# Performance work log

Hardware: AMD Instinct MI355X
Metric: run time of the kernel (lower is better)

Reference implementation:

```python
import jax, jax.numpy as jnp
import numpy as np

N = 50000
H = 8          # heads
C = 10         # out channels per head
F_IN = 128
NEG_SLOPE = 0.2


def _glorot(key, shape, fan_in):
    return jax.random.normal(key, shape, dtype=jnp.float32) / np.sqrt(fan_in)


def setup_inputs() -> dict:
    key = jax.random.key(0)
    ks = jax.random.split(key, 16)
    x = jax.random.normal(ks[0], (N, F_IN), dtype=jnp.float32)
    edge_index = jax.random.randint(ks[1], (2, 1600000), 0, N, dtype=jnp.int64)
    inp = {"x": x, "edge_index": edge_index}
    dims = [F_IN, H * C, H * C]  # input dim of each of the 3 layers
    k = 2
    for i, din in enumerate(dims):
        inp[f"Wl{i}"] = _glorot(ks[k + 0], (din, H * C), din)
        inp[f"Wr{i}"] = _glorot(ks[k + 1], (din, H * C), din)
        inp[f"att{i}"] = _glorot(ks[k + 2], (H, C), C)
        inp[f"b{i}"] = jnp.zeros((H * C,), dtype=jnp.float32)
        k += 3
    return inp


def gatv2_layer(x, Wl, Wr, att, b, src, dst):
    # GATv2Conv (PyG defaults): separate lin_l/lin_r, e = att . leaky_relu(xl_j + xr_i),
    # segment softmax over incoming edges, scatter-add of alpha * xl_j, concat heads + bias.
    n = x.shape[0]
    xl = (x @ Wl).reshape(n, H, C)
    xr = (x @ Wr).reshape(n, H, C)
    e = jax.nn.leaky_relu(xl[src] + xr[dst], NEG_SLOPE)      # [E, H, C]
    score = jnp.einsum('ehc,hc->eh', e, att)                 # [E, H]
    smax = jax.ops.segment_max(score, dst, num_segments=n)   # [N, H]
    ex = jnp.exp(score - smax[dst])
    denom = jax.ops.segment_sum(ex, dst, num_segments=n)
    alpha = ex / (denom[dst] + 1e-16)                        # [E, H]
    out = jax.ops.segment_sum(alpha[:, :, None] * xl[src], dst, num_segments=n)
    return out.reshape(n, H * C) + b


def reference(x, edge_index, Wl0, Wr0, att0, b0, Wl1, Wr1, att1, b1, Wl2, Wr2, att2, b2):
    n = x.shape[0]
    # add_self_loops=True (PyG default)
    loop = jnp.arange(n, dtype=edge_index.dtype)
    src = jnp.concatenate([edge_index[0], loop])
    dst = jnp.concatenate([edge_index[1], loop])
    params = [(Wl0, Wr0, att0, b0), (Wl1, Wr1, att1, b1), (Wl2, Wr2, att2, b2)]
    for Wl, Wr, att, b in params:
        x = jax.nn.elu(gatv2_layer(x, Wl, Wr, att, b, src, dst))
    return x
```

## Files before the change

kernel.cpp:

```cpp
#include <hip/hip_runtime.h>
#include <hip/hip_bf16.h>
#include <hip/hip_fp16.h>

#define N_NODES 50000
#define HEADS 8
#define CHANS 10
#define HC 80
#define PADH 12
#define PHL 96
#define F_IN 128
#define E_EDGES 1600000
#define E_TOT (E_EDGES + N_NODES)
#define NEG_SLOPE 0.2f
#define NBUCK 3125
#define NCHUNK 128
#define CHUNK ((E_TOT + NCHUNK - 1) / NCHUNK)
#define XS_STRIDE 40
#define WS_STRIDE 40

typedef _Float16 f16x8 __attribute__((ext_vector_type(8)));
typedef float f32x4 __attribute__((ext_vector_type(4)));

#if __has_builtin(__builtin_amdgcn_fdot2) && __has_builtin(__builtin_elementwise_max)
#define USE_PK 1
typedef _Float16 h2 __attribute__((ext_vector_type(2)));
#else
#define USE_PK 0
#endif

__device__ inline void load_edge(const void* ei, int is64, int e, int& src, int& dst) {
    if (e < E_EDGES) {
        if (is64) {
            src = ((const int*)ei)[2 * e];
            dst = ((const int*)ei)[2 * (E_EDGES + e)];
        } else {
            src = ((const int*)ei)[e];
            dst = ((const int*)ei)[E_EDGES + e];
        }
    } else {
        src = dst = e - E_EDGES;
    }
}

__device__ inline int load_dst(const void* ei, int is64, int e) {
    if (e < E_EDGES) {
        if (is64) return ((const int*)ei)[2 * (E_EDGES + e)];
        return ((const int*)ei)[E_EDGES + e];
    }
    return e - E_EDGES;
}

__device__ inline int detect_is64(const void* ei, int tid, int* s_flag) {
    if (tid < 64) {
        const int* p = (const int*)ei;
        bool ok = (p[2 * tid + 1] == 0) && (p[2 * (tid + 64) + 1] == 0);
        unsigned long long m = __ballot(ok);
        if (tid == 0) *s_flag = (m == ~0ull) ? 1 : 0;
    }
    return 0;
}

__global__ __launch_bounds__(256) void hist_wconv_kernel(
        const void* ei, int* __restrict__ hist, int* __restrict__ bcount,
        const float* __restrict__ Wl0, const float* __restrict__ Wr0,
        const float* __restrict__ Wl1, const float* __restrict__ Wr1,
        const float* __restrict__ Wl2, const float* __restrict__ Wr2,
        __half* __restrict__ wt) {
    int blk = blockIdx.x;
    int tid = threadIdx.x;
    if (blk >= NCHUNK) {
        if (tid < 128) {
            int g = blk - NCHUNK;
            int layer = g / 160, c = g - layer * 160;
            int kp = tid;
            const float* Wl = (layer == 0) ? Wl0 : (layer == 1) ? Wl1 : Wl2;
            const float* Wr = (layer == 0) ? Wr0 : (layer == 1) ? Wr1 : Wr2;
            const float* W = (c < 80) ? Wl : Wr;
            int cc = (c < 80) ? c : c - 80;
            float v = 0.f;
            if (layer == 0) {
                if (kp < F_IN) v = W[kp * 80 + cc];
            } else {
                int hh = kp / PADH, c2 = kp - hh * PADH;
                if (kp < PHL && c2 < CHANS)
                    v = W[(hh * CHANS + c2) * 80 + cc];
            }
            wt[(size_t)g * 128 + kp] = __float2half_rn(v);
        }
        return;
    }
    __shared__ int h[NBUCK];
    __shared__ int s_is64;
    for (int i = tid; i < NBUCK; i += 256) h[i] = 0;
    detect_is64(ei, tid, &s_is64);
    __syncthreads();
    int is64 = s_is64;
    int e0 = blk * CHUNK, e1 = min(e0 + CHUNK, E_TOT);
    for (int e = e0 + tid; e < e1; e += 4 * 256) {
        int d[4]; int cnt = 0;
        #pragma unroll
        for (int u = 0; u < 4; u++) {
            int ee = e + u * 256;
            if (ee < e1) { d[u] = load_dst(ei, is64, ee); cnt = u + 1; }
        }
        #pragma unroll
        for (int u = 0; u < 4; u++)
            if (u < cnt) atomicAdd(&h[d[u] >> 4], 1);
    }
    __syncthreads();
    for (int i = tid; i < NBUCK; i += 256) {
        int v = h[i];
        int old = v ? atomicAdd(&bcount[i], v) : 0;
        hist[blk * NBUCK + i] = old;
    }
}

__global__ void scan_total_kernel(const int* __restrict__ total, int* __restrict__ bbase) {
    __shared__ int wsum[16];
    __shared__ int wpre[16];
    __shared__ int carry;
    int tid = threadIdx.x;
    int lane = tid & 63, w = tid >> 6;
    if (tid == 0) carry = 0;
    __syncthreads();
    for (int base = 0; base < NBUCK; base += 1024) {
        int idx = base + tid;
        int v = (idx < NBUCK) ? total[idx] : 0;
        int sv = v;
        #pragma unroll
        for (int off = 1; off < 64; off <<= 1) {
            int t = __shfl_up(sv, off, 64);
            if (lane >= off) sv += t;
        }
        if (lane == 63) wsum[w] = sv;
        __syncthreads();
        if (w == 0) {
            int s = (lane < 16) ? wsum[lane] : 0;
            #pragma unroll
            for (int off = 1; off < 16; off <<= 1) {
                int t = __shfl_up(s, off, 64);
                if (lane >= off) s += t;
            }
            if (lane < 16) wpre[lane] = s;
        }
        __syncthreads();
        int pre = carry + ((w > 0) ? wpre[w - 1] : 0);
        if (idx < NBUCK) bbase[idx] = pre + sv - v;
        __syncthreads();
        if (tid == 0) carry += wpre[15];
        __syncthreads();
    }
}

__global__ __launch_bounds__(256) void scatter_sort_kernel(
        const void* ei, const int* __restrict__ hist, const int* __restrict__ bbase,
        int* __restrict__ tmp) {
    __shared__ int cur[NBUCK];
    __shared__ int s_is64;
    int tid = threadIdx.x;
    int blk = blockIdx.x;
    for (int i = tid; i < NBUCK; i += 256)
        cur[i] = bbase[i] + hist[blk * NBUCK + i];
    detect_is64(ei, tid, &s_is64);
    __syncthreads();
    int is64 = s_is64;
    int e0 = blk * CHUNK, e1 = min(e0 + CHUNK, E_TOT);
    for (int e = e0 + tid; e < e1; e += 4 * 256) {
        int s[4], d[4]; int cnt = 0;
        #pragma unroll
        for (int u = 0; u < 4; u++) {
            int ee = e + u * 256;
            if (ee < e1) { load_edge(ei, is64, ee, s[u], d[u]); cnt = u + 1; }
        }
        #pragma unroll
        for (int u = 0; u < 4; u++) {
            if (u < cnt) {
                int pos = atomicAdd(&cur[d[u] >> 4], 1);
                tmp[pos] = (s[u] << 4) | (d[u] & 15);
            }
        }
    }
}

__global__ __launch_bounds__(256) void node_sort_kernel(
        const int* __restrict__ tmp, const int* __restrict__ bbase,
        const int* __restrict__ total,
        int* __restrict__ adj, int* __restrict__ nstart, int* __restrict__ deg) {
    __shared__ int h16[16];
    __shared__ int st16[16];
    __shared__ int cur16[16];
    int tid = threadIdx.x;
    int b = blockIdx.x;
    int base = bbase[b];
    int n = total[b];
    if (tid < 16) h16[tid] = 0;
    __syncthreads();
    for (int k = tid; k < n; k += 256)
        atomicAdd(&h16[tmp[base + k] & 15], 1);
    __syncthreads();
    if (tid == 0) {
        int run = 0;
        #pragma unroll
        for (int c = 0; c < 16; c++) { st16[c] = run; cur16[c] = run; run += h16[c]; }
    }
    __syncthreads();
    for (int k = tid; k < n; k += 256) {
        int p = tmp[base + k];
        int pos = atomicAdd(&cur16[p & 15], 1);
        adj[base + pos] = p >> 4;
    }
    if (tid < 16) {
        nstart[b * 16 + tid] = base + st16[tid];
        deg[b * 16 + tid] = h16[tid];
    }
}

__global__ __launch_bounds__(256) void deghist_kernel(
        const int* __restrict__ deg, int* __restrict__ dh) {
    __shared__ int h[256];
    h[threadIdx.x] = 0;
    __syncthreads();
    int i = blockIdx.x * 256 + threadIdx.x;
    if (i < N_NODES) atomicAdd(&h[min(deg[i], 255)], 1);
    __syncthreads();
    if (h[threadIdx.x]) atomicAdd(&dh[threadIdx.x], h[threadIdx.x]);
}

__global__ void degscan_kernel(const int* __restrict__ dh, int* __restrict__ dcur) {
    __shared__ int s[256];
    int tid = threadIdx.x;
    int idx = 255 - tid;
    int own = dh[idx];
    s[tid] = own;
    __syncthreads();
    for (int off = 1; off < 256; off <<= 1) {
        int t = (tid >= off) ? s[tid - off] : 0;
        __syncthreads();
        s[tid] += t;
        __syncthreads();
    }
    dcur[idx] = s[tid] - own;
}

__global__ __launch_bounds__(256) void degscatter_kernel(
        const int* __restrict__ deg, int* __restrict__ dcur, int* __restrict__ perm) {
    __shared__ int h[256];
    __shared__ int res[256];
    __shared__ int lc[256];
    int tid = threadIdx.x;
    h[tid] = 0; lc[tid] = 0;
    __syncthreads();
    int i = blockIdx.x * 256 + tid;
    int d = (i < N_NODES) ? min(deg[i], 255) : -1;
    if (d >= 0) atomicAdd(&h[d], 1);
    __syncthreads();
    res[tid] = h[tid] ? atomicAdd(&dcur[tid], h[tid]) : 0;
    __syncthreads();
    if (d >= 0) {
        int off = atomicAdd(&lc[d], 1);
        perm[res[d] + off] = i;
    }
}

__global__ __launch_bounds__(256) void gemm_mfma_kernel(
        const void* __restrict__ xin, int in_fp16, int nkt,
        const __half* __restrict__ wt,
        __half* __restrict__ xlh, float* __restrict__ xr) {
    __shared__ __half xs[128 * XS_STRIDE];
    __shared__ __half ws[160 * WS_STRIDE];
    int tid = threadIdx.x;
    int n0 = blockIdx.x * 128;
    int w = tid >> 6, lane = tid & 63;
    int quad = lane >> 4, r = lane & 15;

    f32x4 acc[2][10];
    #pragma unroll
    for (int nt = 0; nt < 2; nt++)
        #pragma unroll
        for (int t = 0; t < 10; t++) acc[nt][t] = (f32x4){0.f, 0.f, 0.f, 0.f};

    int snode = tid >> 1;
    int sk = (tid & 1) * 16;
    int sg = n0 + snode;

    for (int kt = 0; kt < nkt; kt++) {
        f16x8 xv0 = (f16x8){0, 0, 0, 0, 0, 0, 0, 0}, xv1 = xv0;
        if (sg < N_NODES) {
            if (in_fp16) {
                const uint4* p = (const uint4*)((const __half*)xin + (size_t)sg * PHL + kt * 32 + sk);
                xv0 = __builtin_bit_cast(f16x8, p[0]);
                xv1 = __builtin_bit_cast(f16x8, p[1]);
            } else {
                const float4* p = (const float4*)((const float*)xin + (size_t)sg * F_IN + kt * 32 + sk);
                float4 f0 = p[0], f1 = p[1], f2 = p[2], f3 = p[3];
                xv0[0] = (_Float16)f0.x; xv0[1] = (_Float16)f0.y;
                xv0[2] = (_Float16)f0.z; xv0[3] = (_Float16)f0.w;
                xv0[4] = (_Float16)f1.x; xv0[5] = (_Float16)f1.y;
                xv0[6] = (_Float16)f1.z; xv0[7] = (_Float16)f1.w;
                xv1[0] = (_Float16)f2.x; xv1[1] = (_Float16)f2.y;
                xv1[2] = (_Float16)f2.z; xv1[3] = (_Float16)f2.w;
                xv1[4] = (_Float16)f3.x; xv1[5] = (_Float16)f3.y;
                xv1[6] = (_Float16)f3.z; xv1[7] = (_Float16)f3.w;
            }
        }
        __syncthreads();
        *(uint4*)(&xs[snode * XS_STRIDE + sk]) = __builtin_bit_cast(uint4, xv0);
        *(uint4*)(&xs[snode * XS_STRIDE + sk + 8]) = __builtin_bit_cast(uint4, xv1);
        for (int u = tid; u < 640; u += 256) {
            int c = u >> 2, k8 = (u & 3) * 8;
            uint4 wv = *(const uint4*)(wt + c * 128 + kt * 32 + k8);
            *(uint4*)(&ws[c * WS_STRIDE + k8]) = wv;
        }
        __syncthreads();
        #pragma unroll
        for (int nt = 0; nt < 2; nt++) {
            f16x8 a = __builtin_bit_cast(f16x8,
                         *(const uint4*)(&xs[(w * 32 + nt * 16 + r) * XS_STRIDE + quad * 8]));
            #pragma unroll
            for (int ct = 0; ct < 10; ct++) {
                f16x8 bf = __builtin_bit_cast(f16x8,
                              *(const uint4*)(&ws[(ct * 16 + r) * WS_STRIDE + quad * 8]));
                acc[nt][ct] = __builtin_amdgcn_mfma_f32_16x16x32_f16(a, bf, acc[nt][ct], 0, 0, 0);
            }
        }
    }
    #pragma unroll
    for (int nt = 0; nt < 2; nt++) {
        #pragma unroll
        for (int ct = 0; ct < 10; ct++) {
            int col = ct * 16 + r;
            #pragma unroll
            for (int reg = 0; reg < 4; reg++) {
                int node = n0 + w * 32 + nt * 16 + quad * 4 + reg;
                if (node < N_NODES) {
                    float v = acc[nt][ct][reg];
                    if (col < 80) {
                        int hh = col / 10, cc = col - hh * 10;
                        xlh[(size_t)node * PHL + hh * PADH + cc] = __float2half_rn(v);
                    } else {
                        xr[(size_t)node * HC + (col - 80)] = v;
                    }
                }
            }
        }
    }
}

__device__ inline void cvt10(uint2 a, uint2 b, uint2 c, float* v) {
    __half2 h;
    h = *(__half2*)&a.x; v[0] = __low2float(h); v[1] = __high2float(h);
    h = *(__half2*)&a.y; v[2] = __low2float(h); v[3] = __high2float(h);
    h = *(__half2*)&b.x; v[4] = __low2float(h); v[5] = __high2float(h);
    h = *(__half2*)&b.y; v[6] = __low2float(h); v[7] = __high2float(h);
    h = *(__half2*)&c.x; v[8] = __low2float(h); v[9] = __high2float(h);
}

__global__ __launch_bounds__(256, 4) void agg_kernel(
        const __half* __restrict__ xlh, const float* __restrict__ xr,
        const float* __restrict__ att, const float* __restrict__ bias,
        const int* __restrict__ nstart, const int* __restrict__ deg,
        const int* __restrict__ adj, const int* __restrict__ perm,
        __half* __restrict__ ybuf, float* __restrict__ yout) {
    int tid = threadIdx.x;
    int b = blockIdx.x;
    int h = tid & 7;
    int split = (tid >> 3) & 1;
    int i_local = tid >> 4;
    int node = perm[b * 16 + i_local];

    int s0 = nstart[node];
    int dg = deg[node];
    int cnt0 = (dg + 1) >> 1;
    int cnt = split ? (dg - cnt0) : cnt0;
    int k0 = s0 + split * cnt0;

#if USE_PK
    h2 xrh[5], atth[5];
    #pragma unroll
    for (int p = 0; p < 5; p++) {
        xrh[p] = (h2){(_Float16)xr[(size_t)node * HC + h * CHANS + 2 * p],
                      (_Float16)xr[(size_t)node * HC + h * CHANS + 2 * p + 1]};
        atth[p] = (h2){(_Float16)att[h * CHANS + 2 * p],
                       (_Float16)att[h * CHANS + 2 * p + 1]};
    }
    const h2 k02 = {(_Float16)NEG_SLOPE, (_Float16)NEG_SLOPE};
    auto score_pk = [&](const unsigned int* wv) {
        float s = 0.f;
        #pragma unroll
        for (int p = 0; p < 5; p++) {
            h2 v = __builtin_bit_cast(h2, wv[p]);
            h2 t = v + xrh[p];
            h2 tl = __builtin_elementwise_max(t, t * k02);
            s = __builtin_amdgcn_fdot2(tl, atth[p], s, false);
        }
        return s;
    };

    float m = -1e30f, l = 0.f;
    h2 acc[5];
    #pragma unroll
    for (int p = 0; p < 5; p++) acc[p] = (h2){(_Float16)0.f, (_Float16)0.f};

    int kk = 0;
    for (; kk + 8 <= cnt; kk += 8) {
        unsigned int w[8][5];
        #pragma unroll
        for (int r = 0; r < 8; r++) {
            int j = adj[k0 + kk + r];
            const uint2* p = (const uint2*)(xlh + (size_t)j * PHL + h * PADH);
            uint2 a = p[0], bq = p[1], cq = p[2];
            w[r][0] = a.x; w[r][1] = a.y; w[r][2] = bq.x; w[r][3] = bq.y; w[r][4] = cq.x;
        }
        float sc[8];
        #pragma unroll
        for (int r = 0; r < 8; r++) sc[r] = score_pk(w[r]);
        float mb = m;
        #pragma unroll
        for (int r = 0; r < 8; r++) mb = fmaxf(mb, sc[r]);
        float scale = __expf(m - mb);
        float ps = 0.f;
        #pragma unroll
        for (int r = 0; r < 8; r++) { sc[r] = __expf(sc[r] - mb); ps += sc[r]; }
        l = l * scale + ps;
        _Float16 sch = (_Float16)scale;
        h2 sch2 = (h2){sch, sch};
        #pragma unroll
        for (int p = 0; p < 5; p++) acc[p] *= sch2;
        #pragma unroll
        for (int r = 0; r < 8; r++) {
            _Float16 pr = (_Float16)sc[r];
            h2 pr2 = (h2){pr, pr};
            #pragma unroll
            for (int p = 0; p < 5; p++)
                acc[p] += pr2 * __builtin_bit_cast(h2, w[r][p]);
        }
        m = mb;
    }
    for (; kk + 4 <= cnt; kk += 4) {
        unsigned int w[4][5];
        #pragma unroll
        for (int r = 0; r < 4; r++) {
            int j = adj[k0 + kk + r];
            const uint2* p = (const uint2*)(xlh + (size_t)j * PHL + h * PADH);
            uint2 a = p[0], bq = p[1], cq = p[2];
            w[r][0] = a.x; w[r][1] = a.y; w[r][2] = bq.x; w[r][3] = bq.y; w[r][4] = cq.x;
        }
        float sc[4];
        #pragma unroll
        for (int r = 0; r < 4; r++) sc[r] = score_pk(w[r]);
        float mb = m;
        #pragma unroll
        for (int r = 0; r < 4; r++) mb = fmaxf(mb, sc[r]);
        float scale = __expf(m - mb);
        float ps = 0.f;
        #pragma unroll
        for (int r = 0; r < 4; r++) { sc[r] = __expf(sc[r] - mb); ps += sc[r]; }
        l = l * scale + ps;
        _Float16 sch = (_Float16)scale;
        h2 sch2 = (h2){sch, sch};
        #pragma unroll
        for (int p = 0; p < 5; p++) acc[p] *= sch2;
        #pragma unroll
        for (int r = 0; r < 4; r++) {
            _Float16 pr = (_Float16)sc[r];
            h2 pr2 = (h2){pr, pr};
            #pragma unroll
            for (int p = 0; p < 5; p++)
                acc[p] += pr2 * __builtin_bit_cast(h2, w[r][p]);
        }
        m = mb;
    }
    for (; kk < cnt; kk++) {
        int j = adj[k0 + kk];
        const uint2* p = (const uint2*)(xlh + (size_t)j * PHL + h * PADH);
        uint2 a = p[0], bq = p[1], cq = p[2];
        unsigned int w[5] = {a.x, a.y, bq.x, bq.y, cq.x};
        float s = score_pk(w);
        float mn = fmaxf(m, s);
        float scale = __expf(m - mn);
        float pp = __expf(s - mn);
        l = l * scale + pp;
        _Float16 sch = (_Float16)scale, prh = (_Float16)pp;
        h2 sch2 = (h2){sch, sch}, pr2 = (h2){prh, prh};
        #pragma unroll
        for (int p5 = 0; p5 < 5; p5++)
            acc[p5] = acc[p5] * sch2 + pr2 * __builtin_bit_cast(h2, w[p5]);
        m = mn;
    }

    float accm[CHANS];
    float lt;
    {
        float m2 = __shfl_xor(m, 8, 64);
        float l2 = __shfl_xor(l, 8, 64);
        float mn = fmaxf(m, m2);
        float sc1 = __expf(m - mn), sc2 = __expf(m2 - mn);
        lt = l * sc1 + l2 * sc2;
        #pragma unroll
        for (int p = 0; p < 5; p++) {
            unsigned int ua = __builtin_bit_cast(unsigned int, acc[p]);
            unsigned int ub = (unsigned int)__shfl_xor((int)ua, 8, 64);
            h2 va = __builtin_bit_cast(h2, ua);
            h2 vb = __builtin_bit_cast(h2, ub);
            accm[2 * p]     = (float)va[0] * sc1 + (float)vb[0] * sc2;
            accm[2 * p + 1] = (float)va[1] * sc1 + (float)vb[1] * sc2;
        }
    }
#else
    float xr_c[CHANS], att_c[CHANS];
    #pragma unroll
    for (int c = 0; c < CHANS; c++) {
        xr_c[c]  = xr[(size_t)node * HC + h * CHANS + c];
        att_c[c] = att[h * CHANS + c];
    }
    float m = -1e30f, l = 0.f;
    float acc[CHANS];
    #pragma unroll
    for (int c = 0; c < CHANS; c++) acc[c] = 0.f;
    for (int kk = 0; kk < cnt; kk++) {
        int j = adj[k0 + kk];
        const uint2* p = (const uint2*)(xlh + (size_t)j * PHL + h * PADH);
        uint2 a = p[0], bq = p[1], cq = p[2];
        float v[CHANS];
        cvt10(a, bq, cq, v);
        float s = 0.f;
        #pragma unroll
        for (int c = 0; c < CHANS; c++) {
            float t = v[c] + xr_c[c];
            t = (t > 0.f) ? t : NEG_SLOPE * t;
            s += att_c[c] * t;
        }
        float mn = fmaxf(m, s);
        float scale = __expf(m - mn);
        float pp = __expf(s - mn);
        l = l * scale + pp;
        #pragma unroll
        for (int c = 0; c < CHANS; c++) acc[c] = acc[c] * scale + pp * v[c];
        m = mn;
    }
    float accm[CHANS];
    float lt;
    {
        float m2 = __shfl_xor(m, 8, 64);
        float l2 = __shfl_xor(l, 8, 64);
        float mn = fmaxf(m, m2);
        float sc1 = __expf(m - mn), sc2 = __expf(m2 - mn);
        lt = l * sc1 + l2 * sc2;
        #pragma unroll
        for (int c = 0; c < CHANS; c++) {
            float a2 = __shfl_xor(acc[c], 8, 64);
            accm[c] = acc[c] * sc1 + a2 * sc2;
        }
    }
#endif

    if (split == 0) {
        float inv = 1.f / (lt + 1e-16f);
        float z[CHANS];
        #pragma unroll
        for (int c = 0; c < CHANS; c++) {
            float t = accm[c] * inv + bias[h * CHANS + c];
            z[c] = (t > 0.f) ? t : (__expf(t) - 1.f);
        }
        if (yout) {
            #pragma unroll
            for (int c = 0; c < CHANS; c++)
                yout[(size_t)node * HC + h * CHANS + c] = z[c];
        } else {
            __half2 h0 = __halves2half2(__float2half_rn(z[0]), __float2half_rn(z[1]));
            __half2 h1 = __halves2half2(__float2half_rn(z[2]), __float2half_rn(z[3]));
            __half2 h2v = __halves2half2(__float2half_rn(z[4]), __float2half_rn(z[5]));
            __half2 h3 = __halves2half2(__float2half_rn(z[6]), __float2half_rn(z[7]));
            __half2 h4 = __halves2half2(__float2half_rn(z[8]), __float2half_rn(z[9]));
            __half2 h5 = __halves2half2(__half(0.f), __half(0.f));
            uint2* dst = (uint2*)(ybuf + (size_t)node * PHL + h * PADH);
            dst[0] = make_uint2(*(unsigned*)&h0, *(unsigned*)&h1);
            dst[1] = make_uint2(*(unsigned*)&h2v, *(unsigned*)&h3);
            dst[2] = make_uint2(*(unsigned*)&h4, *(unsigned*)&h5);
        }
    }
}

extern "C" void kernel_launch(void* const* d_in, const int* in_sizes, int n_in,
                              void* d_out, int out_size, void* d_ws, size_t ws_size,
                              hipStream_t stream) {
    const float* x_in = (const float*)d_in[0];
    const void*  ei   = d_in[1];
    const float* Wl[3] = {(const float*)d_in[2], (const float*)d_in[6],  (const float*)d_in[10]};
    const float* Wr[3] = {(const float*)d_in[3], (const float*)d_in[7],  (const float*)d_in[11]};
    const float* At[3] = {(const float*)d_in[4], (const float*)d_in[8],  (const float*)d_in[12]};
    const float* Bi[3] = {(const float*)d_in[5], (const float*)d_in[9],  (const float*)d_in[13]};
    float* out = (float*)d_out;

    char* ws = (char*)d_ws;
    size_t off = 0;
    auto alloc = [&](size_t bytes) {
        void* p = ws + off;
        off += (bytes + 255) & ~(size_t)255;
        return p;
    };
    __half* xlh   = (__half*)alloc((size_t)N_NODES * PHL * sizeof(__half));
    float*  xr    = (float*)alloc((size_t)N_NODES * HC * sizeof(float));
    __half* buf16 = (__half*)alloc((size_t)N_NODES * PHL * sizeof(__half));
    __half* wt    = (__half*)alloc((size_t)3 * 160 * 128 * sizeof(__half));
    int*   tmp    = (int*)alloc((size_t)E_TOT * sizeof(int));
    int*   adj    = (int*)alloc((size_t)E_TOT * sizeof(int));
    int*   hist   = (int*)alloc((size_t)NCHUNK * NBUCK * sizeof(int));
    int*   bcount = (int*)alloc((size_t)NBUCK * sizeof(int));
    int*   dh     = (int*)alloc(256 * sizeof(int));
    int*   bbase  = (int*)alloc((size_t)NBUCK * sizeof(int));
    int*   nstart = (int*)alloc((size_t)N_NODES * sizeof(int));
    int*   deg    = (int*)alloc((size_t)N_NODES * sizeof(int));
    int*   perm   = (int*)alloc((size_t)N_NODES * sizeof(int));
    int*   dcur   = (int*)alloc(256 * sizeof(int));

    hipMemsetAsync(bcount, 0, (size_t)((char*)dh - (char*)bcount) + 1024, stream);
    hist_wconv_kernel<<<NCHUNK + 480, 256, 0, stream>>>(
        ei, hist, bcount, Wl[0], Wr[0], Wl[1], Wr[1], Wl[2], Wr[2], wt);
    scan_total_kernel<<<1, 1024, 0, stream>>>(bcount, bbase);
    scatter_sort_kernel<<<NCHUNK, 256, 0, stream>>>(ei, hist, bbase, tmp);
    node_sort_kernel<<<NBUCK, 256, 0, stream>>>(tmp, bbase, bcount, adj, nstart, deg);
    int nblocks = (N_NODES + 255) / 256;
    deghist_kernel<<<nblocks, 256, 0, stream>>>(deg, dh);
    degscan_kernel<<<1, 256, 0, stream>>>(dh, dcur);
    degscatter_kernel<<<nblocks, 256, 0, stream>>>(deg, dcur, perm);

    int gemm_blocks = (N_NODES + 127) / 128;
    const void* cur = (const void*)x_in;
    int in_fp16 = 0;
    for (int layer = 0; layer < 3; layer++) {
        int nkt = (layer == 0) ? 4 : 3;
        gemm_mfma_kernel<<<gemm_blocks, 256, 0, stream>>>(
            cur, in_fp16, nkt, wt + (size_t)layer * 160 * 128, xlh, xr);
        __half* ybuf = (layer == 2) ? nullptr : buf16;
        float*  yout = (layer == 2) ? out : nullptr;
        agg_kernel<<<NBUCK, 256, 0, stream>>>(xlh, xr, At[layer], Bi[layer],
                                              nstart, deg, adj, perm, ybuf, yout);
        cur = (const void*)buf16;
        in_fp16 = 1;
    }
}
```

Before: 343.6 us.

## Drop per-head padding in fp16 features and overlap layer-0 GEMM with histogram

The fp16 feature rows shrink from 96 to 80 halves by removing the per-head padding from 10 to 12 channels. This cuts the bytes touched by the gather in the aggregation kernel and the GEMM input reads, at the cost of narrower 4-byte loads instead of 8-byte vector loads. Weight conversion moves to its own small kernel. The layer-0 GEMM tiles now run as extra blocks of the edge-histogram kernel, sharing its shared-memory buffer, so the two overlap. The degree scan is folded into the degree-scatter kernel, with each block redoing the 256-entry scan, which removes one launch.

```diff
diff --git a/kernel.cpp b/kernel.cpp
--- a/kernel.cpp
+++ b/kernel.cpp
@@ -6,8 +6,7 @@
 #define HEADS 8
 #define CHANS 10
 #define HC 80
-#define PADH 12
-#define PHL 96
+#define PHL 80
 #define F_IN 128
 #define E_EDGES 1600000
 #define E_TOT (E_EDGES + N_NODES)
@@ -15,6 +14,7 @@
 #define NBUCK 3125
 #define NCHUNK 128
 #define CHUNK ((E_TOT + NCHUNK - 1) / NCHUNK)
+#define GEMM_TILES ((N_NODES + 127) / 128)
 #define XS_STRIDE 40
 #define WS_STRIDE 40
 
@@ -60,37 +60,118 @@
     return 0;
 }
 
-__global__ __launch_bounds__(256) void hist_wconv_kernel(
+__global__ void wconv_kernel(const float* __restrict__ Wl0, const float* __restrict__ Wr0,
+                             const float* __restrict__ Wl1, const float* __restrict__ Wr1,
+                             const float* __restrict__ Wl2, const float* __restrict__ Wr2,
+                             __half* __restrict__ wt) {
+    int g = blockIdx.x;
+    int layer = g / 160, c = g - layer * 160;
+    int kp = threadIdx.x;
+    const float* Wl = (layer == 0) ? Wl0 : (layer == 1) ? Wl1 : Wl2;
+    const float* Wr = (layer == 0) ? Wr0 : (layer == 1) ? Wr1 : Wr2;
+    const float* W = (c < 80) ? Wl : Wr;
+    int cc = (c < 80) ? c : c - 80;
+    int din = (layer == 0) ? F_IN : HC;
+    float v = (kp < din) ? W[kp * 80 + cc] : 0.f;
+    wt[(size_t)g * 128 + kp] = __float2half_rn(v);
+}
+
+__device__ __forceinline__ void gemm_tile_body(
+        int tile, const void* __restrict__ xin, int in_fp16, int nkt,
+        const __half* __restrict__ wt,
+        __half* __restrict__ xlh, float* __restrict__ xr,
+        __half* xs, __half* ws) {
+    int tid = threadIdx.x;
+    int n0 = tile * 128;
+    int w = tid >> 6, lane = tid & 63;
+    int quad = lane >> 4, r = lane & 15;
+
+    f32x4 acc[2][10];
+    #pragma unroll
+    for (int nt = 0; nt < 2; nt++)
+        #pragma unroll
+        for (int t = 0; t < 10; t++) acc[nt][t] = (f32x4){0.f, 0.f, 0.f, 0.f};
+
+    int snode = tid >> 1;
+    int sk = (tid & 1) * 16;
+    int sg = n0 + snode;
+
+    for (int kt = 0; kt < nkt; kt++) {
+        f16x8 xv0 = (f16x8){0, 0, 0, 0, 0, 0, 0, 0}, xv1 = xv0;
+        if (sg < N_NODES) {
+            if (in_fp16) {
+                int g0 = kt * 32 + sk;
+                const uint4* p = (const uint4*)((const __half*)xin + (size_t)sg * PHL + g0);
+                if (g0 < PHL)     xv0 = __builtin_bit_cast(f16x8, p[0]);
+                if (g0 + 8 < PHL) xv1 = __builtin_bit_cast(f16x8, p[1]);
+            } else {
+                const float4* p = (const float4*)((const float*)xin + (size_t)sg * F_IN + kt * 32 + sk);
+                float4 f0 = p[0], f1 = p[1], f2 = p[2], f3 = p[3];
+                xv0[0] = (_Float16)f0.x; xv0[1] = (_Float16)f0.y;
+                xv0[2] = (_Float16)f0.z; xv0[3] = (_Float16)f0.w;
+                xv0[4] = (_Float16)f1.x; xv0[5] = (_Float16)f1.y;
+                xv0[6] = (_Float16)f1.z; xv0[7] = (_Float16)f1.w;
+                xv1[0] = (_Float16)f2.x; xv1[1] = (_Float16)f2.y;
+                xv1[2] = (_Float16)f2.z; xv1[3] = (_Float16)f2.w;
+                xv1[4] = (_Float16)f3.x; xv1[5] = (_Float16)f3.y;
+                xv1[6] = (_Float16)f3.z; xv1[7] = (_Float16)f3.w;
+            }
+        }
+        __syncthreads();
+        *(uint4*)(&xs[snode * XS_STRIDE + sk]) = __builtin_bit_cast(uint4, xv0);
+        *(uint4*)(&xs[snode * XS_STRIDE + sk + 8]) = __builtin_bit_cast(uint4, xv1);
+        for (int u = tid; u < 640; u += 256) {
+            int c = u >> 2, k8 = (u & 3) * 8;
+            uint4 wv = *(const uint4*)(wt + c * 128 + kt * 32 + k8);
+            *(uint4*)(&ws[c * WS_STRIDE + k8]) = wv;
+        }
+        __syncthreads();
+        #pragma unroll
+        for (int nt = 0; nt < 2; nt++) {
+            f16x8 a = __builtin_bit_cast(f16x8,
+                         *(const uint4*)(&xs[(w * 32 + nt * 16 + r) * XS_STRIDE + quad * 8]));
+            #pragma unroll
+            for (int ct = 0; ct < 10; ct++) {
+                f16x8 bf = __builtin_bit_cast(f16x8,
+                              *(const uint4*)(&ws[(ct * 16 + r) * WS_STRIDE + quad * 8]));
+                acc[nt][ct] = __builtin_amdgcn_mfma_f32_16x16x32_f16(a, bf, acc[nt][ct], 0, 0, 0);
+            }
+        }
+    }
+    __syncthreads();
+    #pragma unroll
+    for (int nt = 0; nt < 2; nt++) {
+        #pragma unroll
+        for (int ct = 0; ct < 10; ct++) {
+            int col = ct * 16 + r;
+            #pragma unroll
+            for (int reg = 0; reg < 4; reg++) {
+                int node = n0 + w * 32 + nt * 16 + quad * 4 + reg;
+                if (node < N_NODES) {
+                    float v = acc[nt][ct][reg];
+                    if (col < 80) xlh[(size_t)node * PHL + col] = __float2half_rn(v);
+                    else          xr[(size_t)node * HC + (col - 80)] = v;
+                }
+            }
+        }
+    }
+}
+
+__global__ __launch_bounds__(256) void hist_gemm0_kernel(
         const void* ei, int* __restrict__ hist, int* __restrict__ bcount,
-        const float* __restrict__ Wl0, const float* __restrict__ Wr0,
-        const float* __restrict__ Wl1, const float* __restrict__ Wr1,
-        const float* __restrict__ Wl2, const float* __restrict__ Wr2,
-        __half* __restrict__ wt) {
+        const float* __restrict__ x_in, const __half* __restrict__ wt0,
+        __half* __restrict__ xlh, float* __restrict__ xr) {
+    __shared__ __align__(16) char smem[23056];
+    __shared__ int s_is64;
     int blk = blockIdx.x;
     int tid = threadIdx.x;
     if (blk >= NCHUNK) {
-        if (tid < 128) {
-            int g = blk - NCHUNK;
-            int layer = g / 160, c = g - layer * 160;
-            int kp = tid;
-            const float* Wl = (layer == 0) ? Wl0 : (layer == 1) ? Wl1 : Wl2;
-            const float* Wr = (layer == 0) ? Wr0 : (layer == 1) ? Wr1 : Wr2;
-            const float* W = (c < 80) ? Wl : Wr;
-            int cc = (c < 80) ? c : c - 80;
-            float v = 0.f;
-            if (layer == 0) {
-                if (kp < F_IN) v = W[kp * 80 + cc];
-            } else {
-                int hh = kp / PADH, c2 = kp - hh * PADH;
-                if (kp < PHL && c2 < CHANS)
-                    v = W[(hh * CHANS + c2) * 80 + cc];
-            }
-            wt[(size_t)g * 128 + kp] = __float2half_rn(v);
-        }
+        __half* xs = (__half*)smem;
+        __half* ws = (__half*)(smem + 10240);
+        gemm_tile_body(blk - NCHUNK, x_in, 0, 4, wt0, xlh, xr, xs, ws);
         return;
     }
-    __shared__ int h[NBUCK];
-    __shared__ int s_is64;
+    int* h = (int*)smem;
     for (int i = tid; i < NBUCK; i += 256) h[i] = 0;
     detect_is64(ei, tid, &s_is64);
     __syncthreads();
@@ -226,12 +307,19 @@
     if (h[threadIdx.x]) atomicAdd(&dh[threadIdx.x], h[threadIdx.x]);
 }
 
-__global__ void degscan_kernel(const int* __restrict__ dh, int* __restrict__ dcur) {
+__global__ __launch_bounds__(256) void degscatter_kernel(
+        const int* __restrict__ deg, const int* __restrict__ dh,
+        int* __restrict__ resv, int* __restrict__ perm) {
+    __shared__ int sbase[256];
     __shared__ int s[256];
+    __shared__ int h[256];
+    __shared__ int res[256];
+    __shared__ int lc[256];
     int tid = threadIdx.x;
     int idx = 255 - tid;
     int own = dh[idx];
     s[tid] = own;
+    h[tid] = 0; lc[tid] = 0;
     __syncthreads();
     for (int off = 1; off < 256; off <<= 1) {
         int t = (tid >= off) ? s[tid - off] : 0;
@@ -239,26 +327,17 @@
         s[tid] += t;
         __syncthreads();
     }
-    dcur[idx] = s[tid] - own;
-}
-
-__global__ __launch_bounds__(256) void degscatter_kernel(
-        const int* __restrict__ deg, int* __restrict__ dcur, int* __restrict__ perm) {
-    __shared__ int h[256];
-    __shared__ int res[256];
-    __shared__ int lc[256];
-    int tid = threadIdx.x;
-    h[tid] = 0; lc[tid] = 0;
+    sbase[idx] = s[tid] - own;
     __syncthreads();
     int i = blockIdx.x * 256 + tid;
     int d = (i < N_NODES) ? min(deg[i], 255) : -1;
     if (d >= 0) atomicAdd(&h[d], 1);
     __syncthreads();
-    res[tid] = h[tid] ? atomicAdd(&dcur[tid], h[tid]) : 0;
+    res[tid] = h[tid] ? atomicAdd(&resv[tid], h[tid]) : 0;
     __syncthreads();
     if (d >= 0) {
         int off = atomicAdd(&lc[d], 1);
-        perm[res[d] + off] = i;
+        perm[sbase[d] + res[d] + off] = i;
     }
 }
 
@@ -268,91 +347,7 @@
         __half* __restrict__ xlh, float* __restrict__ xr) {
     __shared__ __half xs[128 * XS_STRIDE];
     __shared__ __half ws[160 * WS_STRIDE];
-    int tid = threadIdx.x;
-    int n0 = blockIdx.x * 128;
-    int w = tid >> 6, lane = tid & 63;
-    int quad = lane >> 4, r = lane & 15;
-
-    f32x4 acc[2][10];
-    #pragma unroll
-    for (int nt = 0; nt < 2; nt++)
-        #pragma unroll
-        for (int t = 0; t < 10; t++) acc[nt][t] = (f32x4){0.f, 0.f, 0.f, 0.f};
-
-    int snode = tid >> 1;
-    int sk = (tid & 1) * 16;
-    int sg = n0 + snode;
-
-    for (int kt = 0; kt < nkt; kt++) {
-        f16x8 xv0 = (f16x8){0, 0, 0, 0, 0, 0, 0, 0}, xv1 = xv0;
-        if (sg < N_NODES) {
-            if (in_fp16) {
-                const uint4* p = (const uint4*)((const __half*)xin + (size_t)sg * PHL + kt * 32 + sk);
-                xv0 = __builtin_bit_cast(f16x8, p[0]);
-                xv1 = __builtin_bit_cast(f16x8, p[1]);
-            } else {
-                const float4* p = (const float4*)((const float*)xin + (size_t)sg * F_IN + kt * 32 + sk);
-                float4 f0 = p[0], f1 = p[1], f2 = p[2], f3 = p[3];
-                xv0[0] = (_Float16)f0.x; xv0[1] = (_Float16)f0.y;
-                xv0[2] = (_Float16)f0.z; xv0[3] = (_Float16)f0.w;
-                xv0[4] = (_Float16)f1.x; xv0[5] = (_Float16)f1.y;
-                xv0[6] = (_Float16)f1.z; xv0[7] = (_Float16)f1.w;
-                xv1[0] = (_Float16)f2.x; xv1[1] = (_Float16)f2.y;
-                xv1[2] = (_Float16)f2.z; xv1[3] = (_Float16)f2.w;
-                xv1[4] = (_Float16)f3.x; xv1[5] = (_Float16)f3.y;
-                xv1[6] = (_Float16)f3.z; xv1[7] = (_Float16)f3.w;
-            }
-        }
-        __syncthreads();
-        *(uint4*)(&xs[snode * XS_STRIDE + sk]) = __builtin_bit_cast(uint4, xv0);
-        *(uint4*)(&xs[snode * XS_STRIDE + sk + 8]) = __builtin_bit_cast(uint4, xv1);
-        for (int u = tid; u < 640; u += 256) {
-            int c = u >> 2, k8 = (u & 3) * 8;
-            uint4 wv = *(const uint4*)(wt + c * 128 + kt * 32 + k8);
-            *(uint4*)(&ws[c * WS_STRIDE + k8]) = wv;
-        }
-        __syncthreads();
-        #pragma unroll
-        for (int nt = 0; nt < 2; nt++) {
-            f16x8 a = __builtin_bit_cast(f16x8,
-                         *(const uint4*)(&xs[(w * 32 + nt * 16 + r) * XS_STRIDE + quad * 8]));
-            #pragma unroll
-            for (int ct = 0; ct < 10; ct++) {
-                f16x8 bf = __builtin_bit_cast(f16x8,
-                              *(const uint4*)(&ws[(ct * 16 + r) * WS_STRIDE + quad * 8]));
-                acc[nt][ct] = __builtin_amdgcn_mfma_f32_16x16x32_f16(a, bf, acc[nt][ct], 0, 0, 0);
-            }
-        }
-    }
-    #pragma unroll
-    for (int nt = 0; nt < 2; nt++) {
-        #pragma unroll
-        for (int ct = 0; ct < 10; ct++) {
-            int col = ct * 16 + r;
-            #pragma unroll
-            for (int reg = 0; reg < 4; reg++) {
-                int node = n0 + w * 32 + nt * 16 + quad * 4 + reg;
-                if (node < N_NODES) {
-                    float v = acc[nt][ct][reg];
-                    if (col < 80) {
-                        int hh = col / 10, cc = col - hh * 10;
-                        xlh[(size_t)node * PHL + hh * PADH + cc] = __float2half_rn(v);
-                    } else {
-                        xr[(size_t)node * HC + (col - 80)] = v;
-                    }
-                }
-            }
-        }
-    }
-}
-
-__device__ inline void cvt10(uint2 a, uint2 b, uint2 c, float* v) {
-    __half2 h;
-    h = *(__half2*)&a.x; v[0] = __low2float(h); v[1] = __high2float(h);
-    h = *(__half2*)&a.y; v[2] = __low2float(h); v[3] = __high2float(h);
-    h = *(__half2*)&b.x; v[4] = __low2float(h); v[5] = __high2float(h);
-    h = *(__half2*)&b.y; v[6] = __low2float(h); v[7] = __high2float(h);
-    h = *(__half2*)&c.x; v[8] = __low2float(h); v[9] = __high2float(h);
+    gemm_tile_body(blockIdx.x, xin, in_fp16, nkt, wt, xlh, xr, xs, ws);
 }
 
 __global__ __launch_bounds__(256, 4) void agg_kernel(
@@ -407,9 +402,9 @@
         #pragma unroll
         for (int r = 0; r < 8; r++) {
             int j = adj[k0 + kk + r];
-            const uint2* p = (const uint2*)(xlh + (size_t)j * PHL + h * PADH);
-            uint2 a = p[0], bq = p[1], cq = p[2];
-            w[r][0] = a.x; w[r][1] = a.y; w[r][2] = bq.x; w[r][3] = bq.y; w[r][4] = cq.x;
+            const unsigned int* p = (const unsigned int*)(xlh + (size_t)j * PHL + h * CHANS);
+            #pragma unroll
+            for (int q = 0; q < 5; q++) w[r][q] = p[q];
         }
         float sc[8];
         #pragma unroll
@@ -441,9 +436,9 @@
         #pragma unroll
         for (int r = 0; r < 4; r++) {
             int j = adj[k0 + kk + r];
-            const uint2* p = (const uint2*)(xlh + (size_t)j * PHL + h * PADH);
-            uint2 a = p[0], bq = p[1], cq = p[2];
-            w[r][0] = a.x; w[r][1] = a.y; w[r][2] = bq.x; w[r][3] = bq.y; w[r][4] = cq.x;
+            const unsigned int* p = (const unsigned int*)(xlh + (size_t)j * PHL + h * CHANS);
+            #pragma unroll
+            for (int q = 0; q < 5; q++) w[r][q] = p[q];
         }
         float sc[4];
         #pragma unroll
@@ -472,9 +467,8 @@
     }
     for (; kk < cnt; kk++) {
         int j = adj[k0 + kk];
-        const uint2* p = (const uint2*)(xlh + (size_t)j * PHL + h * PADH);
-        uint2 a = p[0], bq = p[1], cq = p[2];
-        unsigned int w[5] = {a.x, a.y, bq.x, bq.y, cq.x};
+        const unsigned int* p = (const unsigned int*)(xlh + (size_t)j * PHL + h * CHANS);
+        unsigned int w[5] = {p[0], p[1], p[2], p[3], p[4]};
         float s = score_pk(w);
         float mn = fmaxf(m, s);
         float scale = __expf(m - mn);
@@ -519,10 +513,10 @@
     for (int c = 0; c < CHANS; c++) acc[c] = 0.f;
     for (int kk = 0; kk < cnt; kk++) {
         int j = adj[k0 + kk];
-        const uint2* p = (const uint2*)(xlh + (size_t)j * PHL + h * PADH);
-        uint2 a = p[0], bq = p[1], cq = p[2];
+        const __half* p = xlh + (size_t)j * PHL + h * CHANS;
         float v[CHANS];
-        cvt10(a, bq, cq, v);
+        #pragma unroll
+        for (int c = 0; c < CHANS; c++) v[c] = __half2float(p[c]);
         float s = 0.f;
         #pragma unroll
         for (int c = 0; c < CHANS; c++) {
@@ -567,16 +561,13 @@
             for (int c = 0; c < CHANS; c++)
                 yout[(size_t)node * HC + h * CHANS + c] = z[c];
         } else {
-            __half2 h0 = __halves2half2(__float2half_rn(z[0]), __float2half_rn(z[1]));
-            __half2 h1 = __halves2half2(__float2half_rn(z[2]), __float2half_rn(z[3]));
-            __half2 h2v = __halves2half2(__float2half_rn(z[4]), __float2half_rn(z[5]));
-            __half2 h3 = __halves2half2(__float2half_rn(z[6]), __float2half_rn(z[7]));
-            __half2 h4 = __halves2half2(__float2half_rn(z[8]), __float2half_rn(z[9]));
-            __half2 h5 = __halves2half2(__half(0.f), __half(0.f));
-            uint2* dst = (uint2*)(ybuf + (size_t)node * PHL + h * PADH);
-            dst[0] = make_uint2(*(unsigned*)&h0, *(unsigned*)&h1);
-            dst[1] = make_uint2(*(unsigned*)&h2v, *(unsigned*)&h3);
-            dst[2] = make_uint2(*(unsigned*)&h4, *(unsigned*)&h5);
+            unsigned int* dst = (unsigned int*)(ybuf + (size_t)node * PHL + h * CHANS);
+            #pragma unroll
+            for (int p = 0; p < 5; p++) {
+                __half2 hp = __halves2half2(__float2half_rn(z[2 * p]),
+                                            __float2half_rn(z[2 * p + 1]));
+                dst[p] = *(unsigned int*)&hp;
+            }
         }
     }
 }
@@ -608,35 +599,32 @@
     int*   hist   = (int*)alloc((size_t)NCHUNK * NBUCK * sizeof(int));
     int*   bcount = (int*)alloc((size_t)NBUCK * sizeof(int));
     int*   dh     = (int*)alloc(256 * sizeof(int));
+    int*   resv   = (int*)alloc(256 * sizeof(int));
     int*   bbase  = (int*)alloc((size_t)NBUCK * sizeof(int));
     int*   nstart = (int*)alloc((size_t)N_NODES * sizeof(int));
     int*   deg    = (int*)alloc((size_t)N_NODES * sizeof(int));
     int*   perm   = (int*)alloc((size_t)N_NODES * sizeof(int));
-    int*   dcur   = (int*)alloc(256 * sizeof(int));
-
-    hipMemsetAsync(bcount, 0, (size_t)((char*)dh - (char*)bcount) + 1024, stream);
-    hist_wconv_kernel<<<NCHUNK + 480, 256, 0, stream>>>(
-        ei, hist, bcount, Wl[0], Wr[0], Wl[1], Wr[1], Wl[2], Wr[2], wt);
+
+    hipMemsetAsync(bcount, 0, (size_t)((char*)resv - (char*)bcount) + 1024, stream);
+    wconv_kernel<<<480, 128, 0, stream>>>(Wl[0], Wr[0], Wl[1], Wr[1], Wl[2], Wr[2], wt);
+    hist_gemm0_kernel<<<NCHUNK + GEMM_TILES, 256, 0, stream>>>(
+        ei, hist, bcount, x_in, wt, xlh, xr);
     scan_total_kernel<<<1, 1024, 0, stream>>>(bcount, bbase);
     scatter_sort_kernel<<<NCHUNK, 256, 0, stream>>>(ei, hist, bbase, tmp);
     node_sort_kernel<<<NBUCK, 256, 0, stream>>>(tmp, bbase, bcount, adj, nstart, deg);
     int nblocks = (N_NODES + 255) / 256;
     deghist_kernel<<<nblocks, 256, 0, stream>>>(deg, dh);
-    degscan_kernel<<<1, 256, 0, stream>>>(dh, dcur);
-    degscatter_kernel<<<nblocks, 256, 0, stream>>>(deg, dcur, perm);
-
-    int gemm_blocks = (N_NODES + 127) / 128;
-    const void* cur = (const void*)x_in;
-    int in_fp16 = 0;
+    degscatter_kernel<<<nblocks, 256, 0, stream>>>(deg, dh, resv, perm);
+
+    const void* cur = (const void*)buf16;
     for (int layer = 0; layer < 3; layer++) {
-        int nkt = (layer == 0) ? 4 : 3;
-        gemm_mfma_kernel<<<gemm_blocks, 256, 0, stream>>>(
-            cur, in_fp16, nkt, wt + (size_t)layer * 160 * 128, xlh, xr);
+        if (layer > 0) {
+            gemm_mfma_kernel<<<GEMM_TILES, 256, 0, stream>>>(
+                cur, 1, 3, wt + (size_t)layer * 160 * 128, xlh, xr);
+        }
         __half* ybuf = (layer == 2) ? nullptr : buf16;
         float*  yout = (layer == 2) ? out : nullptr;
         agg_kernel<<<NBUCK, 256, 0, stream>>>(xlh, xr, At[layer], Bi[layer],
                                               nstart, deg, adj, perm, ybuf, yout);
-        cur = (const void*)buf16;
-        in_fp16 = 1;
-    }
-}
+    }
+}
```

Result: faster. 320.9 us (-6.6%).
